# Kernel optimization log

Hardware: AMD Instinct MI355X
Metric: run time of the kernel (lower is better)

The kernel has to match this reference:

```python
import jax, jax.numpy as jnp
import numpy as np
import math

NLAT, NLON, LMAX, MMAX = 128, 256, 50, 50
K = 3  # three_nn

# ---- precompute: Clenshaw-Curtis quadrature (torch_harmonics 'equiangular') ----
def _cc_nodes_weights(n):
    Nn = n - 1
    theta = np.pi * np.arange(n) / Nn
    v = np.zeros(n)
    for k in range(1, Nn // 2 + 1):
        b = 1.0 if 2 * k == Nn else 2.0
        v += b * np.cos(2 * k * theta) / (4 * k * k - 1)
    w = (2.0 / Nn) * (1.0 - v)
    w[0] *= 0.5
    w[-1] *= 0.5
    return np.cos(theta), w

# ---- precompute: orthonormal associated Legendre P_l^m(cos theta), csphase ----
def _legpoly(lmax, mmax, cost):
    sint = np.sqrt(np.clip(1.0 - cost ** 2, 0.0, None))
    p = np.zeros((mmax, lmax, cost.shape[0]))
    pmm = np.full(cost.shape[0], np.sqrt(1.0 / (4.0 * np.pi)))
    for m in range(mmax):
        if m > 0:
            pmm = -pmm * np.sqrt((2.0 * m + 1.0) / (2.0 * m)) * sint
        p[m, m] = pmm
        if m + 1 < lmax:
            p[m, m + 1] = np.sqrt(2.0 * m + 3.0) * cost * pmm
        for l in range(m + 2, lmax):
            a = np.sqrt((4.0 * l * l - 1.0) / (l * l - m * m))
            b = np.sqrt(((2.0 * l + 1.0) * (l - 1 + m) * (l - 1 - m)) / ((2.0 * l - 3.0) * (l * l - m * m)))
            p[m, l] = a * cost * p[m, l - 1] - b * p[m, l - 2]
    return p

_cost, _w = _cc_nodes_weights(NLAT)
_PCTW = jnp.asarray((_legpoly(LMAX, MMAX, _cost) * _w[None, None, :]).astype(np.float32))  # (mmax,lmax,nlat)

_gx, _gy = np.meshgrid(np.arange(NLAT), np.arange(-NLAT, NLAT), indexing='ij')
_GRID = jnp.asarray((np.stack([_gx.ravel(), _gy.ravel()], -1) / NLAT * np.pi).astype(np.float32))  # (M,2)

_RECTW = jnp.asarray(np.exp(-(LMAX - np.arange(1, LMAX + 1)) ** 2 / (2.0 * LMAX ** 2)).astype(np.float32))  # (lmax,)


def to_spherical(coords):
    # coords: (B,N,3) -> r:(B,N), sph:(B,N,2) = [arccos(x/r), azimuth in [0,2pi)]
    sq = coords ** 2
    pn = jnp.sqrt(jnp.flip(jnp.cumsum(jnp.flip(sq, -1), -1), -1))  # pn[...,i] = ||coords[...,i:]||
    r = pn[..., 0]
    phi = jnp.arccos(coords[..., :-2] / pn[..., :-2])
    a = jnp.arccos(coords[..., -2] / pn[..., -2])
    phi_final = a + (2.0 * math.pi - 2.0 * a) * (coords[..., -1] < 0)
    return r, jnp.concatenate([phi, phi_final[..., None]], axis=-1)


def interp_to_grid(coords):
    # spherical transform + 3-NN (squared dists) + distance-weighted interpolation onto the lat/lon grid
    r, sph = to_spherical(coords)
    sph = sph.at[..., 1].add(-math.pi)
    # brute-force pairwise squared distances grid(M,2) vs sph(B,N,2): (B,M,N)
    d2 = (jnp.sum(_GRID ** 2, -1)[None, :, None] + jnp.sum(sph ** 2, -1)[:, None, :]
          - 2.0 * jnp.einsum('md,bnd->bmn', _GRID, sph))
    _, idx = jax.lax.top_k(-jax.lax.stop_gradient(d2), K)  # (B,M,K), ascending distance
    sel = jax.vmap(lambda s, i: s[i])(sph, idx)            # (B,M,K,2)
    fsel = jax.vmap(lambda f, i: f[i])(r, idx)             # (B,M,K)
    dk = jnp.sum((_GRID[None, :, None, :] - sel) ** 2, -1)  # recompute selected sq-dists (differentiable)
    w = dk / jnp.sum(dk, -1, keepdims=True)                # weights = dist / sum(dist), as in source
    return jnp.sum(fsel * w, -1).reshape(-1, NLAT, NLON)


def sht_real(x):
    # RealSHT (equiangular, ortho): rfft(norm='forward')*2pi, then Legendre*quadrature einsum; real part only
    xf = jnp.fft.rfft(x, axis=-1)[..., :MMAX] * (2.0 * math.pi / NLON)
    return jnp.einsum('bkm,mlk->blm', jnp.real(xf).astype(jnp.float32), _PCTW)  # (B,lmax,mmax)


def setup_inputs() -> dict:
    key = jax.random.key(0)
    k1, k2 = jax.random.split(key)
    pred = jax.random.normal(k1, (2, 2048, 3), dtype=jnp.float32)
    target = jax.random.normal(k2, (2, 2048, 3), dtype=jnp.float32)
    return {"pred": pred, "target": target}


def reference(pred, target):
    pc = sht_real(interp_to_grid(pred))
    tc = sht_real(interp_to_grid(target))
    return jnp.mean(jnp.sum((pc - tc) ** 2 * _RECTW[None, :, None], axis=(1, 2)))
```

## Files before the change

### kernel.cpp

```cpp
#include <hip/hip_runtime.h>
#include <math.h>

#define PI_D 3.14159265358979323846
#define PIF  3.14159265358979323846f
#define NLAT 128
#define NLON 256
#define LMAX 50
#define MMAX 50
#define NPTS 2048
#define NBT 16
#define NBA 32
#define NBIN (NBT * NBA)
#define WBIN 0.19634954084936207f
#define INVW 5.092958178940651f
#define BIG 1e30f
#define KMASK 0xFFFFF800u

__device__ float g_pctwT[(size_t)LMAX * NLAT * MMAX];
__device__ float g_fre[(size_t)4 * NLAT * MMAX];

__device__ __forceinline__ void insert3(float kf, float& k0, float& k1, float& k2) {
    float n1 = __builtin_amdgcn_fmed3f(kf, k0, k1);
    float n2 = __builtin_amdgcn_fmed3f(kf, k1, k2);
    k0 = fminf(kf, k0);
    k1 = n1;
    k2 = n2;
}

__device__ __forceinline__ float mkkey(float gt, float gl, float2 tl, int idx) {
    float dt = gt - tl.x, dl = gl - tl.y;
    float d = fmaf(dt, dt, dl * dl);
    return __uint_as_float((__float_as_uint(d) & KMASK) | (unsigned)idx);
}

__global__ __launch_bounds__(256) void fused_main(
    const float* __restrict__ pred, const float* __restrict__ tgt,
    float* __restrict__ out) {

    __shared__ float2 s_btl[NPTS];
    __shared__ float  s_br[NPTS];
    __shared__ int    s_cnt[NBIN];
    __shared__ int    s_off[NBIN + 1];
    __shared__ float  s_row[NLON];
    __shared__ float  s_part[256];

    int bid = blockIdx.x;
    int t = threadIdx.x;

    if (bid >= 512) {
        int k = bid - 512;
        int m = t;
        if (k == 0 && m == 0) out[0] = 0.0f;
        if (m >= MMAX) return;

        double thd = PI_D * (double)k / 127.0;
        float cost = (float)cos(thd);
        float sint = (float)sin(thd);

        float c2 = (float)cos(2.0 * thd);
        float two_c2 = 2.0f * c2;
        float cp = 1.0f, cc = c2, v = 0.0f;
        for (int tt = 1; tt <= 63; ++tt) {
            v += 2.0f * cc / (float)(4 * tt * tt - 1);
            float cn = two_c2 * cc - cp;
            cp = cc;
            cc = cn;
        }
        float w = (2.0f / 127.0f) * (1.0f - v);
        if (k == 0 || k == 127) w *= 0.5f;

        float pmm = sqrtf(1.0f / (4.0f * PIF));
        for (int i = 1; i <= m; ++i)
            pmm = -pmm * sqrtf((2.0f * (float)i + 1.0f) / (2.0f * (float)i)) * sint;

        float* o = g_pctwT + (size_t)k * MMAX + m;
        for (int l = 0; l < m; ++l) o[(size_t)l * NLAT * MMAX] = 0.0f;
        o[(size_t)m * NLAT * MMAX] = pmm * w;
        float plm2 = pmm, plm1 = 0.0f;
        if (m + 1 < LMAX) {
            plm1 = sqrtf(2.0f * (float)m + 3.0f) * cost * pmm;
            o[(size_t)(m + 1) * NLAT * MMAX] = plm1 * w;
        }
        for (int l = m + 2; l < LMAX; ++l) {
            float fl = (float)l;
            float denom = fl * fl - (float)(m * m);
            float a = sqrtf((4.0f * fl * fl - 1.0f) / denom);
            float b = sqrtf(((2.0f * fl + 1.0f) * (float)(l - 1 + m) * (float)(l - 1 - m)) /
                            ((2.0f * fl - 3.0f) * denom));
            float p = a * cost * plm1 - b * plm2;
            o[(size_t)l * NLAT * MMAX] = p * w;
            plm2 = plm1;
            plm1 = p;
        }
        return;
    }

    int f = bid >> 7;
    int lat = bid & 127;
    const float* src = ((f < 2) ? pred : tgt) + (size_t)(f & 1) * NPTS * 3;

    for (int i = t; i < NBIN; i += 256) s_cnt[i] = 0;
    __syncthreads();

    float pth[8], paz[8], pr[8];
    int pbin[8];
#pragma unroll
    for (int i = 0; i < 8; ++i) {
        int n = t + 256 * i;
        float x = src[3 * n], y = src[3 * n + 1], z = src[3 * n + 2];
        float s1 = z * z;
        float s2 = s1 + y * y;
        float s3 = s2 + x * x;
        float r = sqrtf(s3);
        float rho = sqrtf(s2);
        float th = acosf(x / r);
        float a = acosf(y / rho);
        float az = (z < 0.0f) ? (a + (2.0f * PIF - 2.0f * a)) : a;
        az -= PIF;
        int bt = min(max((int)(th * INVW), 0), NBT - 1);
        int ba = min(max((int)((az + PIF) * INVW), 0), NBA - 1);
        int b = bt * NBA + ba;
        pth[i] = th; paz[i] = az; pr[i] = r; pbin[i] = b;
        atomicAdd(&s_cnt[b], 1);
    }
    __syncthreads();

    if (t == 0) s_off[NBIN] = NPTS;
    if (t < 64) {
        int base = t * 8;
        int loc[8];
        int run = 0;
#pragma unroll
        for (int i = 0; i < 8; ++i) { loc[i] = run; run += s_cnt[base + i]; }
        int x = run;
#pragma unroll
        for (int d = 1; d < 64; d <<= 1) {
            int y = __shfl_up(x, d);
            if (t >= d) x += y;
        }
        int ex = x - run;
#pragma unroll
        for (int i = 0; i < 8; ++i) s_off[base + i] = ex + loc[i];
    }
    __syncthreads();
    for (int i = t; i < NBIN; i += 256) s_cnt[i] = s_off[i];
    __syncthreads();
#pragma unroll
    for (int i = 0; i < 8; ++i) {
        int pos = atomicAdd(&s_cnt[pbin[i]], 1);
        s_btl[pos] = make_float2(pth[i], paz[i]);
        s_br[pos] = pr[i];
    }
    __syncthreads();

    int j = t;
    float gt = (float)((double)lat * PI_D / 128.0);
    float gl = (float)(((double)j - 128.0) * PI_D / 128.0);
    float glp = gl + PIF;
    int bt0 = lat >> 3;
    int ba0 = j >> 3;

    auto scan_seg = [&](int i, int i1, float& q0, float& q1, float& q2) {
        for (; i + 4 <= i1; i += 4) {
            float2 a0 = s_btl[i];
            float2 a1 = s_btl[i + 1];
            float2 a2 = s_btl[i + 2];
            float2 a3 = s_btl[i + 3];
            insert3(mkkey(gt, gl, a0, i), q0, q1, q2);
            insert3(mkkey(gt, gl, a1, i + 1), q0, q1, q2);
            insert3(mkkey(gt, gl, a2, i + 2), q0, q1, q2);
            insert3(mkkey(gt, gl, a3, i + 3), q0, q1, q2);
        }
        for (; i < i1; ++i)
            insert3(mkkey(gt, gl, s_btl[i], i), q0, q1, q2);
    };

    float k0 = BIG, k1 = BIG, k2 = BIG;
    {
        int rtl = max(bt0 - 1, 0), rth = min(bt0 + 1, NBT - 1);
        int bal = max(ba0 - 1, 0), bah = min(ba0 + 1, NBA - 1);
        for (int bt = rtl; bt <= rth; ++bt)
            scan_seg(s_off[bt * NBA + bal], s_off[bt * NBA + bah + 1], k0, k1, k2);
    }

    bool done;
    {
        float safe = BIG;
        if (bt0 - 1 > 0)       safe = fminf(safe, gt - (float)(bt0 - 1) * WBIN);
        if (bt0 + 1 < NBT - 1) safe = fminf(safe, (float)(bt0 + 2) * WBIN - gt);
        if (ba0 - 1 > 0)       safe = fminf(safe, glp - (float)(ba0 - 1) * WBIN);
        if (ba0 + 1 < NBA - 1) safe = fminf(safe, (float)(ba0 + 2) * WBIN - glp);
        done = (k2 <= safe * safe);
    }

    for (int R = 2; R <= 31; ++R) {
        if (__all(done)) break;
        if (!done) {
            int btl = bt0 - R, bth = bt0 + R;
            int lo = max(btl, 0), hi = min(bth, NBT - 1);
            int bal = max(ba0 - R, 0), bah = min(ba0 + R, NBA - 1);
            for (int bt = lo; bt <= hi; ++bt) {
                if (bt == btl || bt == bth) {
                    scan_seg(s_off[bt * NBA + bal], s_off[bt * NBA + bah + 1], k0, k1, k2);
                } else {
                    if (ba0 - R >= 0) {
                        int b = bt * NBA + ba0 - R;
                        scan_seg(s_off[b], s_off[b + 1], k0, k1, k2);
                    }
                    if (ba0 + R <= NBA - 1) {
                        int b = bt * NBA + ba0 + R;
                        scan_seg(s_off[b], s_off[b + 1], k0, k1, k2);
                    }
                }
            }
            float safe = BIG;
            if (bt0 - R > 0)       safe = fminf(safe, gt - (float)(bt0 - R) * WBIN);
            if (bt0 + R < NBT - 1) safe = fminf(safe, (float)(bt0 + R + 1) * WBIN - gt);
            if (ba0 - R > 0)       safe = fminf(safe, glp - (float)(ba0 - R) * WBIN);
            if (ba0 + R < NBA - 1) safe = fminf(safe, (float)(ba0 + R + 1) * WBIN - glp);
            if (k2 <= safe * safe) done = true;
        }
    }

    {
        int i0 = __float_as_uint(k0) & 0x7FF;
        int i1 = __float_as_uint(k1) & 0x7FF;
        int i2 = __float_as_uint(k2) & 0x7FF;
        float2 p0 = s_btl[i0];
        float2 p1 = s_btl[i1];
        float2 p2 = s_btl[i2];
        float dt0 = gt - p0.x, dl0 = gl - p0.y;
        float dt1 = gt - p1.x, dl1 = gl - p1.y;
        float dt2 = gt - p2.x, dl2 = gl - p2.y;
        float d0 = fmaf(dt0, dt0, dl0 * dl0);
        float d1 = fmaf(dt1, dt1, dl1 * dl1);
        float d2 = fmaf(dt2, dt2, dl2 * dl2);
        float s = d0 + d1 + d2;
        s_row[j] = (d0 * s_br[i0] + d1 * s_br[i1] + d2 * s_br[i2]) / s;
    }
    __syncthreads();

    {
        int q = t >> 6;
        int mm = t & 63;
        if (mm < MMAX) {
            int bs = q * 64;
            const float W0 = 2.0f * PIF / 256.0f;
            float cphi2 = 2.0f * __cosf(W0 * (float)mm);
            float acc = 0.0f;
#pragma unroll
            for (int seg = 0; seg < 4; ++seg) {
                int i0 = bs + seg * 16;
                float c0 = __cosf(W0 * (float)((i0 * mm) & 255));
                float c1 = __cosf(W0 * (float)(((i0 + 1) * mm) & 255));
                acc = fmaf(s_row[i0], c0, acc);
                acc = fmaf(s_row[i0 + 1], c1, acc);
#pragma unroll
                for (int i = 2; i < 16; ++i) {
                    float cn = fmaf(cphi2, c1, -c0);
                    acc = fmaf(s_row[i0 + i], cn, acc);
                    c0 = c1;
                    c1 = cn;
                }
            }
            s_part[q * 64 + mm] = acc;
        }
    }
    __syncthreads();
    if (t < MMAX) {
        int mm = t;
        float v = ((s_part[mm] + s_part[64 + mm]) + (s_part[128 + mm] + s_part[192 + mm])) *
                  (float)(2.0 * PI_D / (double)NLON);
        g_fre[(f * NLAT + lat) * MMAX + mm] = v;
    }
}

__global__ __launch_bounds__(256) void contract_loss(float* __restrict__ out) {
    int b = blockIdx.x / LMAX;
    int l = blockIdx.x % LMAX;
    int mm = threadIdx.x & 63;
    int kq = threadIdx.x >> 6;
    __shared__ float sp[4][64], st_[4][64];
    float pc = 0.0f, tc = 0.0f;
    if (mm < MMAX) {
        const float* pw = g_pctwT + ((size_t)l * NLAT + kq * 32) * MMAX + mm;
        const float* fp = g_fre + ((size_t)b * NLAT + kq * 32) * MMAX + mm;
        const float* ft = g_fre + ((size_t)(2 + b) * NLAT + kq * 32) * MMAX + mm;
#pragma unroll 8
        for (int k = 0; k < 32; ++k) {
            float w = pw[k * MMAX];
            pc += fp[k * MMAX] * w;
            tc += ft[k * MMAX] * w;
        }
    }
    sp[kq][mm] = pc;
    st_[kq][mm] = tc;
    __syncthreads();
    if (threadIdx.x < 64) {
        int m2 = threadIdx.x;
        float pcs = (sp[0][m2] + sp[1][m2]) + (sp[2][m2] + sp[3][m2]);
        float tcs = (st_[0][m2] + st_[1][m2]) + (st_[2][m2] + st_[3][m2]);
        float diff = pcs - tcs;
        double dl_ = (double)(49 - l);
        float rw = (float)exp(-(dl_ * dl_) / 5000.0);
        float contrib = (m2 < MMAX) ? diff * diff * rw * 0.5f : 0.0f;
        for (int off = 32; off > 0; off >>= 1) contrib += __shfl_down(contrib, off);
        if (m2 == 0) atomicAdd(out, contrib);
    }
}

extern "C" void kernel_launch(void* const* d_in, const int* in_sizes, int n_in,
                              void* d_out, int out_size, void* d_ws, size_t ws_size,
                              hipStream_t stream) {
    const float* pred = (const float*)d_in[0];
    const float* tgt = (const float*)d_in[1];
    float* out = (float*)d_out;
    (void)d_ws; (void)ws_size;

    fused_main<<<640, 256, 0, stream>>>(pred, tgt, out);
    contract_loss<<<2 * LMAX, 256, 0, stream>>>(out);
}
```

Before: 84.28 us.

## Split point binning into separate kernel and read bins from global memory

```diff
diff --git a/kernel.cpp b/kernel.cpp
--- a/kernel.cpp
+++ b/kernel.cpp
@@ -16,8 +16,11 @@
 #define BIG 1e30f
 #define KMASK 0xFFFFF800u
 
-__device__ float g_pctwT[(size_t)LMAX * NLAT * MMAX];
-__device__ float g_fre[(size_t)4 * NLAT * MMAX];
+__device__ float2 g_btl[4][NPTS];
+__device__ float  g_br[4][NPTS];
+__device__ int    g_boff[4][NBIN + 1];
+__device__ float  g_pctwT[(size_t)LMAX * NLAT * MMAX];
+__device__ float  g_fre[(size_t)4 * NLAT * MMAX];
 
 __device__ __forceinline__ void insert3(float kf, float& k0, float& k1, float& k2) {
     float n1 = __builtin_amdgcn_fmed3f(kf, k0, k1);
@@ -33,70 +36,14 @@
     return __uint_as_float((__float_as_uint(d) & KMASK) | (unsigned)idx);
 }
 
-__global__ __launch_bounds__(256) void fused_main(
-    const float* __restrict__ pred, const float* __restrict__ tgt,
-    float* __restrict__ out) {
-
-    __shared__ float2 s_btl[NPTS];
-    __shared__ float  s_br[NPTS];
-    __shared__ int    s_cnt[NBIN];
-    __shared__ int    s_off[NBIN + 1];
-    __shared__ float  s_row[NLON];
-    __shared__ float  s_part[256];
-
-    int bid = blockIdx.x;
+__global__ __launch_bounds__(256) void bin_fields(
+    const float* __restrict__ pred, const float* __restrict__ tgt) {
+
+    __shared__ int s_cnt[NBIN];
+    __shared__ int s_off[NBIN + 1];
+
+    int f = blockIdx.x;
     int t = threadIdx.x;
-
-    if (bid >= 512) {
-        int k = bid - 512;
-        int m = t;
-        if (k == 0 && m == 0) out[0] = 0.0f;
-        if (m >= MMAX) return;
-
-        double thd = PI_D * (double)k / 127.0;
-        float cost = (float)cos(thd);
-        float sint = (float)sin(thd);
-
-        float c2 = (float)cos(2.0 * thd);
-        float two_c2 = 2.0f * c2;
-        float cp = 1.0f, cc = c2, v = 0.0f;
-        for (int tt = 1; tt <= 63; ++tt) {
-            v += 2.0f * cc / (float)(4 * tt * tt - 1);
-            float cn = two_c2 * cc - cp;
-            cp = cc;
-            cc = cn;
-        }
-        float w = (2.0f / 127.0f) * (1.0f - v);
-        if (k == 0 || k == 127) w *= 0.5f;
-
-        float pmm = sqrtf(1.0f / (4.0f * PIF));
-        for (int i = 1; i <= m; ++i)
-            pmm = -pmm * sqrtf((2.0f * (float)i + 1.0f) / (2.0f * (float)i)) * sint;
-
-        float* o = g_pctwT + (size_t)k * MMAX + m;
-        for (int l = 0; l < m; ++l) o[(size_t)l * NLAT * MMAX] = 0.0f;
-        o[(size_t)m * NLAT * MMAX] = pmm * w;
-        float plm2 = pmm, plm1 = 0.0f;
-        if (m + 1 < LMAX) {
-            plm1 = sqrtf(2.0f * (float)m + 3.0f) * cost * pmm;
-            o[(size_t)(m + 1) * NLAT * MMAX] = plm1 * w;
-        }
-        for (int l = m + 2; l < LMAX; ++l) {
-            float fl = (float)l;
-            float denom = fl * fl - (float)(m * m);
-            float a = sqrtf((4.0f * fl * fl - 1.0f) / denom);
-            float b = sqrtf(((2.0f * fl + 1.0f) * (float)(l - 1 + m) * (float)(l - 1 - m)) /
-                            ((2.0f * fl - 3.0f) * denom));
-            float p = a * cost * plm1 - b * plm2;
-            o[(size_t)l * NLAT * MMAX] = p * w;
-            plm2 = plm1;
-            plm1 = p;
-        }
-        return;
-    }
-
-    int f = bid >> 7;
-    int lat = bid & 127;
     const float* src = ((f < 2) ? pred : tgt) + (size_t)(f & 1) * NPTS * 3;
 
     for (int i = t; i < NBIN; i += 256) s_cnt[i] = 0;
@@ -144,13 +91,79 @@
     }
     __syncthreads();
     for (int i = t; i < NBIN; i += 256) s_cnt[i] = s_off[i];
+    for (int i = t; i <= NBIN; i += 256) g_boff[f][i] = s_off[i];
     __syncthreads();
 #pragma unroll
     for (int i = 0; i < 8; ++i) {
         int pos = atomicAdd(&s_cnt[pbin[i]], 1);
-        s_btl[pos] = make_float2(pth[i], paz[i]);
-        s_br[pos] = pr[i];
-    }
+        g_btl[f][pos] = make_float2(pth[i], paz[i]);
+        g_br[f][pos] = pr[i];
+    }
+}
+
+__global__ __launch_bounds__(256) void query_pctw(float* __restrict__ out) {
+
+    __shared__ int   s_off[NBIN + 1];
+    __shared__ float s_row[NLON];
+    __shared__ float s_part[256];
+
+    int bid = blockIdx.x;
+    int t = threadIdx.x;
+
+    if (bid >= 512) {
+        int k = bid - 512;
+        int m = t;
+        if (k == 0 && m == 0) out[0] = 0.0f;
+        if (m >= MMAX) return;
+
+        double thd = PI_D * (double)k / 127.0;
+        float cost = (float)cos(thd);
+        float sint = (float)sin(thd);
+
+        float c2 = (float)cos(2.0 * thd);
+        float two_c2 = 2.0f * c2;
+        float cp = 1.0f, cc = c2, v = 0.0f;
+        for (int tt = 1; tt <= 63; ++tt) {
+            v += 2.0f * cc / (float)(4 * tt * tt - 1);
+            float cn = two_c2 * cc - cp;
+            cp = cc;
+            cc = cn;
+        }
+        float w = (2.0f / 127.0f) * (1.0f - v);
+        if (k == 0 || k == 127) w *= 0.5f;
+
+        float pmm = sqrtf(1.0f / (4.0f * PIF));
+        for (int i = 1; i <= m; ++i)
+            pmm = -pmm * sqrtf((2.0f * (float)i + 1.0f) / (2.0f * (float)i)) * sint;
+
+        float* o = g_pctwT + (size_t)k * MMAX + m;
+        for (int l = 0; l < m; ++l) o[(size_t)l * NLAT * MMAX] = 0.0f;
+        o[(size_t)m * NLAT * MMAX] = pmm * w;
+        float plm2 = pmm, plm1 = 0.0f;
+        if (m + 1 < LMAX) {
+            plm1 = sqrtf(2.0f * (float)m + 3.0f) * cost * pmm;
+            o[(size_t)(m + 1) * NLAT * MMAX] = plm1 * w;
+        }
+        for (int l = m + 2; l < LMAX; ++l) {
+            float fl = (float)l;
+            float denom = fl * fl - (float)(m * m);
+            float a = sqrtf((4.0f * fl * fl - 1.0f) / denom);
+            float b = sqrtf(((2.0f * fl + 1.0f) * (float)(l - 1 + m) * (float)(l - 1 - m)) /
+                            ((2.0f * fl - 3.0f) * denom));
+            float p = a * cost * plm1 - b * plm2;
+            o[(size_t)l * NLAT * MMAX] = p * w;
+            plm2 = plm1;
+            plm1 = p;
+        }
+        return;
+    }
+
+    int f = bid >> 7;
+    int lat = bid & 127;
+    const float2* __restrict__ btl = g_btl[f];
+    const float*  __restrict__ br  = g_br[f];
+
+    for (int i = t; i <= NBIN; i += 256) s_off[i] = g_boff[f][i];
     __syncthreads();
 
     int j = t;
@@ -162,17 +175,17 @@
 
     auto scan_seg = [&](int i, int i1, float& q0, float& q1, float& q2) {
         for (; i + 4 <= i1; i += 4) {
-            float2 a0 = s_btl[i];
-            float2 a1 = s_btl[i + 1];
-            float2 a2 = s_btl[i + 2];
-            float2 a3 = s_btl[i + 3];
+            float2 a0 = btl[i];
+            float2 a1 = btl[i + 1];
+            float2 a2 = btl[i + 2];
+            float2 a3 = btl[i + 3];
             insert3(mkkey(gt, gl, a0, i), q0, q1, q2);
             insert3(mkkey(gt, gl, a1, i + 1), q0, q1, q2);
             insert3(mkkey(gt, gl, a2, i + 2), q0, q1, q2);
             insert3(mkkey(gt, gl, a3, i + 3), q0, q1, q2);
         }
         for (; i < i1; ++i)
-            insert3(mkkey(gt, gl, s_btl[i], i), q0, q1, q2);
+            insert3(mkkey(gt, gl, btl[i], i), q0, q1, q2);
     };
 
     float k0 = BIG, k1 = BIG, k2 = BIG;
@@ -196,11 +209,11 @@
     for (int R = 2; R <= 31; ++R) {
         if (__all(done)) break;
         if (!done) {
-            int btl = bt0 - R, bth = bt0 + R;
-            int lo = max(btl, 0), hi = min(bth, NBT - 1);
+            int btl_ = bt0 - R, bth = bt0 + R;
+            int lo = max(btl_, 0), hi = min(bth, NBT - 1);
             int bal = max(ba0 - R, 0), bah = min(ba0 + R, NBA - 1);
             for (int bt = lo; bt <= hi; ++bt) {
-                if (bt == btl || bt == bth) {
+                if (bt == btl_ || bt == bth) {
                     scan_seg(s_off[bt * NBA + bal], s_off[bt * NBA + bah + 1], k0, k1, k2);
                 } else {
                     if (ba0 - R >= 0) {
@@ -226,9 +239,9 @@
         int i0 = __float_as_uint(k0) & 0x7FF;
         int i1 = __float_as_uint(k1) & 0x7FF;
         int i2 = __float_as_uint(k2) & 0x7FF;
-        float2 p0 = s_btl[i0];
-        float2 p1 = s_btl[i1];
-        float2 p2 = s_btl[i2];
+        float2 p0 = btl[i0];
+        float2 p1 = btl[i1];
+        float2 p2 = btl[i2];
         float dt0 = gt - p0.x, dl0 = gl - p0.y;
         float dt1 = gt - p1.x, dl1 = gl - p1.y;
         float dt2 = gt - p2.x, dl2 = gl - p2.y;
@@ -236,7 +249,7 @@
         float d1 = fmaf(dt1, dt1, dl1 * dl1);
         float d2 = fmaf(dt2, dt2, dl2 * dl2);
         float s = d0 + d1 + d2;
-        s_row[j] = (d0 * s_br[i0] + d1 * s_br[i1] + d2 * s_br[i2]) / s;
+        s_row[j] = (d0 * br[i0] + d1 * br[i1] + d2 * br[i2]) / s;
     }
     __syncthreads();
 
@@ -317,6 +330,7 @@
     float* out = (float*)d_out;
     (void)d_ws; (void)ws_size;
 
-    fused_main<<<640, 256, 0, stream>>>(pred, tgt, out);
+    bin_fields<<<4, 256, 0, stream>>>(pred, tgt);
+    query_pctw<<<640, 256, 0, stream>>>(out);
     contract_loss<<<2 * LMAX, 256, 0, stream>>>(out);
 }
```

Measured after the change: 89.42 us. 1.06x slower.
